# Optimization experiments

Hardware: AMD Instinct MI355X
Metric: run time of the kernel (lower is better)

Reference implementation:

```python
import jax, jax.numpy as jnp
import numpy as np

B, T, C = 2, 2048, 2048
N_HEAD, D_HEAD = 16, 128

def setup_inputs() -> dict:
    key = jax.random.key(0)
    k1, k2, k3 = jax.random.split(key, 3)
    x = jax.random.normal(k1, (B, T, C), dtype=jnp.float32)
    # lecun-normal-ish scaling for kernels
    W_attn = jax.random.normal(k2, (C, 3 * C), dtype=jnp.float32) * (1.0 / np.sqrt(C))
    W_proj = jax.random.normal(k3, (C, C), dtype=jnp.float32) * (1.0 / np.sqrt(C))
    return {"x": x, "W_attn": W_attn, "W_proj": W_proj}

def reference(x, W_attn, W_proj):
    Bx, Tx, Cx = x.shape
    # fused qkv projection: (B,T,C) @ (C,3C)
    qkv = x @ W_attn
    q, k, v = jnp.split(qkv, 3, axis=-1)
    # (B, H, T, Dh)
    q = q.reshape(Bx, Tx, N_HEAD, D_HEAD).transpose(0, 2, 1, 3)
    k = k.reshape(Bx, Tx, N_HEAD, D_HEAD).transpose(0, 2, 1, 3)
    v = v.reshape(Bx, Tx, N_HEAD, D_HEAD).transpose(0, 2, 1, 3)
    scale = 1.0 / jnp.sqrt(jnp.asarray(D_HEAD, dtype=x.dtype))
    att = jnp.einsum('bhqd,bhkd->bhqk', q, k) * scale  # (B,H,T,T)
    causal_mask = jnp.tril(jnp.ones((Tx, Tx), dtype=jnp.bool_))[None, None]
    att = jnp.where(causal_mask, att, -jnp.inf)
    att = jax.nn.softmax(att, axis=-1)
    y = jnp.einsum('bhqk,bhkd->bhqd', att, v)
    y = y.transpose(0, 2, 1, 3).reshape(Bx, Tx, Cx)
    return y @ W_proj
```

## Files before the change

kernel.cpp:

```cpp
#include <hip/hip_runtime.h>
#include <hip/hip_bf16.h>
#include <stdint.h>

#define AS1 __attribute__((address_space(1)))
#define AS3 __attribute__((address_space(3)))

typedef __bf16 bf16_t;
typedef __bf16 bf16x8 __attribute__((ext_vector_type(8)));
typedef float f32x4 __attribute__((ext_vector_type(4)));
typedef float f32x16 __attribute__((ext_vector_type(16)));

static constexpr int Bsz = 2, T = 2048, Cdim = 2048, NH = 16, DH = 128;
static constexpr int M  = Bsz * T;
static constexpr int N1 = 3 * Cdim;
static constexpr int K1 = Cdim;

__device__ __forceinline__ unsigned short f2bf(float f) {
  unsigned u = __float_as_uint(f);
  u += 0x7fffu + ((u >> 16) & 1u);
  return (unsigned short)(u >> 16);
}

__device__ __forceinline__ void gload_lds16(const bf16_t* g, void* l) {
  __builtin_amdgcn_global_load_lds((AS1 const void*)g, (AS3 void*)l, 16, 0, 0);
}

__device__ __forceinline__ float ex2(float x) {
  float r; asm("v_exp_f32 %0, %1" : "=v"(r) : "v"(x)); return r;
}
__device__ __forceinline__ unsigned pk2(float a, float b) {
  unsigned r; asm("v_cvt_pk_bf16_f32 %0, %1, %2" : "=v"(r) : "v"(a), "v"(b)); return r;
}

__global__ void cvt_kernel(const float* __restrict__ in, unsigned short* __restrict__ out, int n) {
  int i = (blockIdx.x * blockDim.x + threadIdx.x) * 4;
  if (i >= n) return;
  float4 v = *(const float4*)(in + i);
  ushort4 o;
  o.x = f2bf(v.x); o.y = f2bf(v.y); o.z = f2bf(v.z); o.w = f2bf(v.w);
  *(ushort4*)(out + i) = o;
}

__global__ void transpose_cvt_kernel(const float* __restrict__ in, unsigned short* __restrict__ out,
                                     int K, int N) {
  __shared__ float tile[32][33];
  int n0 = blockIdx.x * 32, k0 = blockIdx.y * 32;
  int tx = threadIdx.x, ty = threadIdx.y;
#pragma unroll
  for (int i = 0; i < 32; i += 8)
    tile[ty + i][tx] = in[(size_t)(k0 + ty + i) * N + n0 + tx];
  __syncthreads();
#pragma unroll
  for (int i = 0; i < 32; i += 8)
    out[(size_t)(n0 + ty + i) * K + k0 + tx] = f2bf(tile[tx][ty + i]);
}

__global__ void vtrans_kernel(const unsigned short* __restrict__ qkv, unsigned short* __restrict__ vt) {
  __shared__ unsigned short tile[32][33];
  int t0 = blockIdx.x * 32, d0 = blockIdx.y * 32, bh = blockIdx.z;
  int b = bh >> 4, h = bh & 15;
  int tx = threadIdx.x, ty = threadIdx.y;
  const unsigned short* src = qkv + (size_t)(b * T) * N1 + 2 * Cdim + h * DH;
#pragma unroll
  for (int i = 0; i < 32; i += 8)
    tile[ty + i][tx] = src[(size_t)(t0 + ty + i) * N1 + d0 + tx];
  __syncthreads();
  unsigned short* dst = vt + ((size_t)bh * DH + d0) * T + t0;
#pragma unroll
  for (int i = 0; i < 32; i += 8)
    dst[(size_t)(ty + i) * T + tx] = tile[tx][ty + i];
}

template <int OUT_BF16>
__global__ __launch_bounds__(512, 4) void gemm_p3(const bf16_t* __restrict__ A,
                                                  const bf16_t* __restrict__ BT,
                                                  void* __restrict__ Cp,
                                                  int Nn, int Kk) {
  constexpr int SLOT = 24576;
  __shared__ __align__(16) char ldsmem[3 * SLOT];
  char* ldsb = ldsmem;

  const int tid = threadIdx.x;
  const int wid = tid >> 6, lane = tid & 63;
  const int lq = lane & 15, lk = lane >> 4;
  const int wr = wid >> 2, wc = wid & 3;

  const int nwg = gridDim.x;
  const int bid = blockIdx.x;
  const int q8 = nwg >> 3;
  const int sw = (bid & 7) * q8 + (bid >> 3);
  const int gx = Nn >> 8;
  const int tn = sw % gx;
  const int tm = sw / gx;

  f32x4 acc[4][4] = {};

  int aoff[4], boff[4];
#pragma unroll
  for (int m = 0; m < 4; ++m) {
    int row = wr * 64 + m * 16 + lq;
    aoff[m] = row * 64 + ((lk * 16) ^ (((row >> 1) & 3) << 4));
  }
#pragma unroll
  for (int n = 0; n < 4; ++n) {
    int brow = wc * 64 + n * 16 + lq;
    boff[n] = 8192 + brow * 64 + ((lk * 16) ^ (((brow >> 1) & 3) << 4));
  }

  const int pA = wid * 1024 + lane * 16;
  const int arow = pA >> 6;
  const int acsw = (pA & 63) ^ (((arow >> 1) & 3) << 4);
  const bf16_t* Ags = A + (size_t)(tm * 128 + arow) * Kk + (acsw >> 1);

  const int pB0 = wid * 1024 + lane * 16;
  const int brow0 = pB0 >> 6;
  const int bcsw0 = (pB0 & 63) ^ (((brow0 >> 1) & 3) << 4);
  const bf16_t* Bgs0 = BT + (size_t)(tn * 256 + brow0) * Kk + (bcsw0 >> 1);

  const int pB1 = 8192 + wid * 1024 + lane * 16;
  const int brow1 = pB1 >> 6;
  const int bcsw1 = (pB1 & 63) ^ (((brow1 >> 1) & 3) << 4);
  const bf16_t* Bgs1 = BT + (size_t)(tn * 256 + brow1) * Kk + (bcsw1 >> 1);

  const int ldsA = wid * 1024;
  const int ldsB0 = 8192 + wid * 1024;
  const int ldsB1 = 16384 + wid * 1024;

  auto stage = [&](int kt, int slot) {
    char* db = ldsb + slot * SLOT;
    gload_lds16(Ags + (size_t)kt * 32, db + ldsA);
    gload_lds16(Bgs0 + (size_t)kt * 32, db + ldsB0);
    gload_lds16(Bgs1 + (size_t)kt * 32, db + ldsB1);
  };

  const int nk = Kk >> 5;

  stage(0, 0); stage(1, 1);
  asm volatile("s_waitcnt vmcnt(3)" ::: "memory");
  __builtin_amdgcn_s_barrier();

#define TILE_BODY(KT, SLOT0, SLOT2, STAGE_EN, VM)                                \
  {                                                                              \
    __builtin_amdgcn_sched_barrier(0);                                           \
    const char* sb = ldsb + (SLOT0) * SLOT;                                      \
    bf16x8 af[4], bfv[4];                                                        \
    _Pragma("unroll") for (int m = 0; m < 4; ++m)                                \
      af[m] = *(const bf16x8*)(sb + aoff[m]);                                    \
    _Pragma("unroll") for (int n = 0; n < 4; ++n)                                \
      bfv[n] = *(const bf16x8*)(sb + boff[n]);                                   \
    if (STAGE_EN) stage((KT) + 2, (SLOT2));                                      \
    __builtin_amdgcn_sched_barrier(0);                                           \
    __builtin_amdgcn_s_barrier();                                                \
    asm volatile("s_waitcnt lgkmcnt(0)" ::: "memory");                           \
    __builtin_amdgcn_sched_barrier(0);                                           \
    __builtin_amdgcn_s_setprio(1);                                               \
    _Pragma("unroll") for (int m = 0; m < 4; ++m)                                \
      _Pragma("unroll") for (int n = 0; n < 4; ++n)                              \
        acc[m][n] =                                                              \
            __builtin_amdgcn_mfma_f32_16x16x32_bf16(af[m], bfv[n], acc[m][n], 0, 0, 0); \
    __builtin_amdgcn_s_setprio(0);                                               \
    __builtin_amdgcn_sched_barrier(0);                                           \
    asm volatile("s_waitcnt vmcnt(" #VM ")" ::: "memory");                       \
    __builtin_amdgcn_s_barrier();                                                \
  }

  {
    int c0 = 0;
    for (int kt = 0; kt < nk - 2; ++kt) {
      const int c2 = (c0 >= 1) ? (c0 - 1) : (c0 + 2);
      TILE_BODY(kt, c0, c2, 1, 3);
      c0 = (c0 >= 2) ? 0 : (c0 + 1);
    }
    TILE_BODY(nk - 2, c0, 0, 0, 0);
    c0 = (c0 >= 2) ? 0 : (c0 + 1);
    TILE_BODY(nk - 1, c0, 0, 0, 0);
  }
#undef TILE_BODY

#pragma unroll
  for (int m = 0; m < 4; ++m)
#pragma unroll
    for (int n = 0; n < 4; ++n)
#pragma unroll
      for (int r = 0; r < 4; ++r) {
        int row = tm * 128 + wr * 64 + m * 16 + lk * 4 + r;
        int col = tn * 256 + wc * 64 + n * 16 + lq;
        if (OUT_BF16)
          ((unsigned short*)Cp)[(size_t)row * Nn + col] = f2bf(acc[m][n][r]);
        else
          ((float*)Cp)[(size_t)row * Nn + col] = acc[m][n][r];
      }
}

__global__ __launch_bounds__(512, 1) void attn_kernel(const bf16_t* __restrict__ qkv,
                                                      const bf16_t* __restrict__ vt,
                                                      unsigned short* __restrict__ y) {
  __shared__ __align__(16) char lds[65536];
  const int tid = threadIdx.x;
  const int wid = tid >> 6, lane = tid & 63;
  const int l31 = lane & 31, hi = lane >> 5;
  const int hi16 = hi << 4;
  const int bh = blockIdx.x;
  const int g = blockIdx.y;
  const int b = bh >> 4, h = bh & 15;
  const float SC2 = 0.12751879868954096f;

  const int grp = (wid < 4) ? g : (15 - g);
  const int qlo = grp * 128 + (wid & 3) * 32;
  const int qidx = qlo + l31;
  const int nt = 2 * (15 - g) + 2;
  const size_t rowbase = (size_t)(b * T) * N1;

  bf16x8 qf[8];
  {
    const bf16_t* Qg = qkv + rowbase + (size_t)qidx * N1 + h * DH + hi * 8;
#pragma unroll
    for (int kk = 0; kk < 8; ++kk) qf[kk] = *(const bf16x8*)(Qg + kk * 16);
  }

  const bf16_t* Kg0 = qkv + rowbase + Cdim + h * DH;
  const bf16_t* Vg0 = vt + (size_t)bh * DH * T;
  const int p0 = wid * 1024 + lane * 16;
  const int p1 = 8192 + wid * 1024 + lane * 16;
  const int kr0 = p0 >> 8, kr1 = p1 >> 8;
  const bf16_t* KsA = Kg0 + (size_t)kr0 * N1 + ((((p0 & 255) ^ ((kr0 & 15) << 4))) >> 1);
  const bf16_t* KsB = Kg0 + (size_t)kr1 * N1 + ((((p1 & 255) ^ ((kr1 & 15) << 4))) >> 1);
  const int vr0 = p0 >> 7, vr1 = p1 >> 7;
  const bf16_t* VsA = Vg0 + (size_t)vr0 * T + ((((p0 & 127) ^ ((vr0 & 7) << 4))) >> 1);
  const bf16_t* VsB = Vg0 + (size_t)vr1 * T + ((((p1 & 127) ^ ((vr1 & 7) << 4))) >> 1);
  const int dstoff = wid * 1024;

  auto stage = [&](int tt) {
    char* Kd = lds + (tt & 1) * 16384;
    char* Vd = lds + 32768 + (tt & 1) * 16384;
    const size_t ko = (size_t)(tt * 64) * N1;
    const int vo = tt * 64;
    gload_lds16(KsA + ko, Kd + dstoff);
    gload_lds16(KsB + ko, Kd + 8192 + dstoff);
    gload_lds16(VsA + vo, Vd + dstoff);
    gload_lds16(VsB + vo, Vd + 8192 + dstoff);
  };

  f32x16 oacc[4] = {};
  float mrow = -1e30f, lrow = 0.f;

  stage(0);
  asm volatile("s_waitcnt vmcnt(0)" ::: "memory");
  __builtin_amdgcn_s_barrier();

  for (int t = 0; t < nt; ++t) {
    const int kv0 = t * 64;
    if (t + 1 < nt) stage(t + 1);

    if (kv0 <= qlo + 31) {
      f32x16 s0 = {}, s1 = {};
      {
        const char* Kb = lds + (t & 1) * 16384;
        const char* krow0 = Kb + l31 * 256;
        const char* krow1 = Kb + (32 + l31) * 256;
        const int sw0 = (l31 & 15) << 4;
        const int sw1 = ((32 + l31) & 15) << 4;
#pragma unroll
        for (int kk = 0; kk < 8; ++kk) {
          bf16x8 kf0 = *(const bf16x8*)(krow0 + ((kk * 32 + hi16) ^ sw0));
          bf16x8 kf1 = *(const bf16x8*)(krow1 + ((kk * 32 + hi16) ^ sw1));
          s0 = __builtin_amdgcn_mfma_f32_32x32x16_bf16(kf0, qf[kk], s0, 0, 0, 0);
          s1 = __builtin_amdgcn_mfma_f32_32x32x16_bf16(kf1, qf[kk], s1, 0, 0, 0);
        }
      }
      float sv[32];
#pragma unroll
      for (int r = 0; r < 16; ++r) { sv[r] = s0[r]; sv[16 + r] = s1[r]; }
      if (kv0 + 63 > qlo) {
#pragma unroll
        for (int r = 0; r < 16; ++r) {
          const int roff = (r & 3) + 8 * (r >> 2);
          if (kv0 + roff + 4 * hi > qidx) sv[r] = -1e30f;
          if (kv0 + 32 + roff + 4 * hi > qidx) sv[16 + r] = -1e30f;
        }
      }
      float mx = sv[0];
#pragma unroll
      for (int i = 1; i < 32; ++i) mx = fmaxf(mx, sv[i]);
      mx = fmaxf(mx, __shfl_xor(mx, 32));
      const float mn = fmaxf(mrow, mx);
      const float osc = ex2((mrow - mn) * SC2);
      mrow = mn;
      const float mn2 = mn * SC2;
#pragma unroll
      for (int db = 0; db < 4; ++db) oacc[db] *= osc;
      float srow = 0.f;
#pragma unroll
      for (int i = 0; i < 32; ++i) {
        float p = ex2(fmaf(sv[i], SC2, -mn2));
        sv[i] = p;
        srow += p;
      }
      srow += __shfl_xor(srow, 32);
      lrow = lrow * osc + srow;
      bf16x8 pb[4];
#pragma unroll
      for (int s4 = 0; s4 < 4; ++s4) {
        const int base = (s4 >> 1) * 16 + (s4 & 1) * 8;
        unsigned x0 = pk2(sv[base + 0], sv[base + 1]);
        unsigned x1 = pk2(sv[base + 2], sv[base + 3]);
        unsigned y0 = pk2(sv[base + 4], sv[base + 5]);
        unsigned y1 = pk2(sv[base + 6], sv[base + 7]);
        unsigned e0 = (unsigned)__shfl_xor((int)(hi ? x0 : y0), 32);
        unsigned e1 = (unsigned)__shfl_xor((int)(hi ? x1 : y1), 32);
        union { unsigned u[4]; bf16x8 v; } pbu;
        pbu.u[0] = hi ? e0 : x0;
        pbu.u[1] = hi ? e1 : x1;
        pbu.u[2] = hi ? y0 : e0;
        pbu.u[3] = hi ? y1 : e1;
        pb[s4] = pbu.v;
      }
      {
        const char* Vb = lds + 32768 + (t & 1) * 16384;
#pragma unroll
        for (int db = 0; db < 4; ++db) {
          const int vrow = db * 32 + l31;
          const char* vr = Vb + vrow * 128;
          const int swv = (vrow & 7) << 4;
#pragma unroll
          for (int s4 = 0; s4 < 4; ++s4) {
            bf16x8 vf = *(const bf16x8*)(vr + ((s4 * 32 + hi16) ^ swv));
            oacc[db] = __builtin_amdgcn_mfma_f32_32x32x16_bf16(vf, pb[s4], oacc[db], 0, 0, 0);
          }
        }
      }
    }

    asm volatile("s_waitcnt vmcnt(0)" ::: "memory");
    __builtin_amdgcn_s_barrier();
  }

  const float inv = 1.0f / lrow;
  char* eb = lds + wid * 8192;
#pragma unroll
  for (int db = 0; db < 4; ++db)
#pragma unroll
    for (int r = 0; r < 16; ++r) {
      const int d = db * 32 + (r & 3) + 8 * (r >> 2) + 4 * hi;
      const int off = l31 * 256 + ((d * 2) ^ ((l31 & 15) << 4));
      *(unsigned short*)(eb + off) = f2bf(oacc[db][r] * inv);
    }
  asm volatile("s_waitcnt lgkmcnt(0)" ::: "memory");
  __builtin_amdgcn_sched_barrier(0);
  {
    unsigned short* yr = y + (size_t)(b * T + qlo + l31) * Cdim + h * DH;
#pragma unroll
    for (int rr = 0; rr < 8; ++rr) {
      const int c = hi * 8 + rr;
      bf16x8 v = *(const bf16x8*)(eb + l31 * 256 + ((c * 16) ^ ((l31 & 15) << 4)));
      *(bf16x8*)(yr + c * 8) = v;
    }
  }
}

extern "C" void kernel_launch(void* const* d_in, const int* in_sizes, int n_in,
                              void* d_out, int out_size, void* d_ws, size_t ws_size,
                              hipStream_t stream) {
  const float* x  = (const float*)d_in[0];
  const float* Wa = (const float*)d_in[1];
  const float* Wp = (const float*)d_in[2];
  float* out = (float*)d_out;
  char* ws = (char*)d_ws;

  size_t o0 = 0;
  size_t o1 = o0 + (size_t)M * K1 * 2;
  size_t o2 = o1 + (size_t)N1 * K1 * 2;
  size_t o3 = o2 + (size_t)M * N1 * 2;
  size_t o4 = o3 + (size_t)M * Cdim * 2;

  unsigned short* xb   = (unsigned short*)(ws + o0);
  unsigned short* WaT  = (unsigned short*)(ws + o1);
  unsigned short* qkvb = (unsigned short*)(ws + o2);
  unsigned short* yb   = (unsigned short*)(ws + o3);
  unsigned short* WpT  = (unsigned short*)(ws + o4);
  unsigned short* vtb  = xb;

  cvt_kernel<<<dim3((M * K1 / 4 + 255) / 256), dim3(256), 0, stream>>>(x, xb, M * K1);
  transpose_cvt_kernel<<<dim3(N1 / 32, K1 / 32), dim3(32, 8), 0, stream>>>(Wa, WaT, K1, N1);
  transpose_cvt_kernel<<<dim3(Cdim / 32, Cdim / 32), dim3(32, 8), 0, stream>>>(Wp, WpT, Cdim, Cdim);

  gemm_p3<1><<<dim3((M / 128) * (N1 / 256)), dim3(512), 0, stream>>>(
      (const bf16_t*)xb, (const bf16_t*)WaT, (void*)qkvb, N1, K1);

  vtrans_kernel<<<dim3(T / 32, DH / 32, Bsz * NH), dim3(32, 8), 0, stream>>>(qkvb, vtb);

  attn_kernel<<<dim3(Bsz * NH, 8), dim3(512), 0, stream>>>(
      (const bf16_t*)qkvb, (const bf16_t*)vtb, yb);

  gemm_p3<0><<<dim3((M / 128) * (Cdim / 256)), dim3(512), 0, stream>>>(
      (const bf16_t*)yb, (const bf16_t*)WpT, (void*)out, Cdim, K1);
}
```

Baseline: 249.6 us.

## Fuse preamble conversions, write V transposed from QKV GEMM, split GEMM tile body

The x conversion and the two weight transpose-conversions are merged into one preamble launch. The QKV GEMM epilogue now writes the V section already transposed, per batch and head, into the V region of qkv, so the separate vtrans kernel goes away and attention reads V^T straight from qkv. The GEMM inner tile is also split into two half-MFMA phases that interleave the A/B LDS reads and global-to-LDS staging, aiming for better overlap. This relies on the V region being laid out as D x T inside the N1-stride buffer, and it adds an extra barrier per k-step.

```diff
diff --git a/kernel.cpp b/kernel.cpp
--- a/kernel.cpp
+++ b/kernel.cpp
@@ -32,46 +32,41 @@
   unsigned r; asm("v_cvt_pk_bf16_f32 %0, %1, %2" : "=v"(r) : "v"(a), "v"(b)); return r;
 }
 
-__global__ void cvt_kernel(const float* __restrict__ in, unsigned short* __restrict__ out, int n) {
-  int i = (blockIdx.x * blockDim.x + threadIdx.x) * 4;
-  if (i >= n) return;
-  float4 v = *(const float4*)(in + i);
-  ushort4 o;
-  o.x = f2bf(v.x); o.y = f2bf(v.y); o.z = f2bf(v.z); o.w = f2bf(v.w);
-  *(ushort4*)(out + i) = o;
-}
-
-__global__ void transpose_cvt_kernel(const float* __restrict__ in, unsigned short* __restrict__ out,
-                                     int K, int N) {
+__global__ __launch_bounds__(256) void preamble_kernel(const float* __restrict__ x,
+                                                       const float* __restrict__ Wa,
+                                                       const float* __restrict__ Wp,
+                                                       unsigned short* __restrict__ xb,
+                                                       unsigned short* __restrict__ WaT,
+                                                       unsigned short* __restrict__ WpT) {
   __shared__ float tile[32][33];
-  int n0 = blockIdx.x * 32, k0 = blockIdx.y * 32;
-  int tx = threadIdx.x, ty = threadIdx.y;
+  const int blk = blockIdx.x;
+  const int tid = threadIdx.x;
+  if (blk < 8192) {
+    int i = blk * 1024 + tid * 4;
+    float4 v = *(const float4*)(x + i);
+    ushort4 o;
+    o.x = f2bf(v.x); o.y = f2bf(v.y); o.z = f2bf(v.z); o.w = f2bf(v.w);
+    *(ushort4*)(xb + i) = o;
+    return;
+  }
+  const float* in;
+  unsigned short* out;
+  int Nn, bi;
+  if (blk < 20480) { in = Wa; out = WaT; Nn = N1;   bi = blk - 8192;  }
+  else             { in = Wp; out = WpT; Nn = Cdim; bi = blk - 20480; }
+  const int ntiles = Nn >> 5;
+  const int n0 = (bi % ntiles) * 32, k0 = (bi / ntiles) * 32;
+  const int tx = tid & 31, ty = tid >> 5;
 #pragma unroll
   for (int i = 0; i < 32; i += 8)
-    tile[ty + i][tx] = in[(size_t)(k0 + ty + i) * N + n0 + tx];
+    tile[ty + i][tx] = in[(size_t)(k0 + ty + i) * Nn + n0 + tx];
   __syncthreads();
 #pragma unroll
   for (int i = 0; i < 32; i += 8)
-    out[(size_t)(n0 + ty + i) * K + k0 + tx] = f2bf(tile[tx][ty + i]);
-}
-
-__global__ void vtrans_kernel(const unsigned short* __restrict__ qkv, unsigned short* __restrict__ vt) {
-  __shared__ unsigned short tile[32][33];
-  int t0 = blockIdx.x * 32, d0 = blockIdx.y * 32, bh = blockIdx.z;
-  int b = bh >> 4, h = bh & 15;
-  int tx = threadIdx.x, ty = threadIdx.y;
-  const unsigned short* src = qkv + (size_t)(b * T) * N1 + 2 * Cdim + h * DH;
-#pragma unroll
-  for (int i = 0; i < 32; i += 8)
-    tile[ty + i][tx] = src[(size_t)(t0 + ty + i) * N1 + d0 + tx];
-  __syncthreads();
-  unsigned short* dst = vt + ((size_t)bh * DH + d0) * T + t0;
-#pragma unroll
-  for (int i = 0; i < 32; i += 8)
-    dst[(size_t)(ty + i) * T + tx] = tile[tx][ty + i];
-}
-
-template <int OUT_BF16>
+    out[(size_t)(n0 + ty + i) * K1 + k0 + tx] = f2bf(tile[tx][ty + i]);
+}
+
+template <int MODE>
 __global__ __launch_bounds__(512, 4) void gemm_p3(const bf16_t* __restrict__ A,
                                                   const bf16_t* __restrict__ BT,
                                                   void* __restrict__ Cp,
@@ -143,21 +138,43 @@
   {                                                                              \
     __builtin_amdgcn_sched_barrier(0);                                           \
     const char* sb = ldsb + (SLOT0) * SLOT;                                      \
-    bf16x8 af[4], bfv[4];                                                        \
-    _Pragma("unroll") for (int m = 0; m < 4; ++m)                                \
-      af[m] = *(const bf16x8*)(sb + aoff[m]);                                    \
+    bf16x8 af0, af1, af2, af3, bfv[4];                                           \
+    af0 = *(const bf16x8*)(sb + aoff[0]);                                        \
+    af1 = *(const bf16x8*)(sb + aoff[1]);                                        \
     _Pragma("unroll") for (int n = 0; n < 4; ++n)                                \
       bfv[n] = *(const bf16x8*)(sb + boff[n]);                                   \
-    if (STAGE_EN) stage((KT) + 2, (SLOT2));                                      \
+    if (STAGE_EN) {                                                              \
+      char* db = ldsb + (SLOT2) * SLOT;                                          \
+      gload_lds16(Ags + (size_t)((KT) + 2) * 32, db + ldsA);                     \
+      gload_lds16(Bgs0 + (size_t)((KT) + 2) * 32, db + ldsB0);                   \
+    }                                                                            \
     __builtin_amdgcn_sched_barrier(0);                                           \
     __builtin_amdgcn_s_barrier();                                                \
     asm volatile("s_waitcnt lgkmcnt(0)" ::: "memory");                           \
     __builtin_amdgcn_sched_barrier(0);                                           \
     __builtin_amdgcn_s_setprio(1);                                               \
-    _Pragma("unroll") for (int m = 0; m < 4; ++m)                                \
-      _Pragma("unroll") for (int n = 0; n < 4; ++n)                              \
-        acc[m][n] =                                                              \
-            __builtin_amdgcn_mfma_f32_16x16x32_bf16(af[m], bfv[n], acc[m][n], 0, 0, 0); \
+    _Pragma("unroll") for (int n = 0; n < 4; ++n) {                              \
+      acc[0][n] = __builtin_amdgcn_mfma_f32_16x16x32_bf16(af0, bfv[n], acc[0][n], 0, 0, 0); \
+      acc[1][n] = __builtin_amdgcn_mfma_f32_16x16x32_bf16(af1, bfv[n], acc[1][n], 0, 0, 0); \
+    }                                                                            \
+    __builtin_amdgcn_s_setprio(0);                                               \
+    __builtin_amdgcn_sched_barrier(0);                                           \
+    __builtin_amdgcn_s_barrier();                                                \
+    af2 = *(const bf16x8*)(sb + aoff[2]);                                        \
+    af3 = *(const bf16x8*)(sb + aoff[3]);                                        \
+    if (STAGE_EN) {                                                              \
+      char* db = ldsb + (SLOT2) * SLOT;                                          \
+      gload_lds16(Bgs1 + (size_t)((KT) + 2) * 32, db + ldsB1);                   \
+    }                                                                            \
+    __builtin_amdgcn_sched_barrier(0);                                           \
+    __builtin_amdgcn_s_barrier();                                                \
+    asm volatile("s_waitcnt lgkmcnt(0)" ::: "memory");                           \
+    __builtin_amdgcn_sched_barrier(0);                                           \
+    __builtin_amdgcn_s_setprio(1);                                               \
+    _Pragma("unroll") for (int n = 0; n < 4; ++n) {                              \
+      acc[2][n] = __builtin_amdgcn_mfma_f32_16x16x32_bf16(af2, bfv[n], acc[2][n], 0, 0, 0); \
+      acc[3][n] = __builtin_amdgcn_mfma_f32_16x16x32_bf16(af3, bfv[n], acc[3][n], 0, 0, 0); \
+    }                                                                            \
     __builtin_amdgcn_s_setprio(0);                                               \
     __builtin_amdgcn_sched_barrier(0);                                           \
     asm volatile("s_waitcnt vmcnt(" #VM ")" ::: "memory");                       \
@@ -177,23 +194,38 @@
   }
 #undef TILE_BODY
 
-#pragma unroll
-  for (int m = 0; m < 4; ++m)
-#pragma unroll
-    for (int n = 0; n < 4; ++n)
-#pragma unroll
-      for (int r = 0; r < 4; ++r) {
-        int row = tm * 128 + wr * 64 + m * 16 + lk * 4 + r;
-        int col = tn * 256 + wc * 64 + n * 16 + lq;
-        if (OUT_BF16)
-          ((unsigned short*)Cp)[(size_t)row * Nn + col] = f2bf(acc[m][n][r]);
-        else
-          ((float*)Cp)[(size_t)row * Nn + col] = acc[m][n][r];
-      }
+  if (MODE == 1 && tn >= 16) {
+    unsigned short* q16 = (unsigned short*)Cp;
+#pragma unroll
+    for (int m = 0; m < 4; ++m)
+#pragma unroll
+      for (int n = 0; n < 4; ++n) {
+        int row = tm * 128 + wr * 64 + m * 16 + lk * 4;
+        int b_ = row >> 11, t0 = row & 2047;
+        int c = tn * 256 - 4096 + wc * 64 + n * 16 + lq;
+        ushort4 o;
+        o.x = f2bf(acc[m][n][0]); o.y = f2bf(acc[m][n][1]);
+        o.z = f2bf(acc[m][n][2]); o.w = f2bf(acc[m][n][3]);
+        *(ushort4*)(q16 + (size_t)(b_ * 2048 + c) * N1 + 4096 + t0) = o;
+      }
+  } else {
+#pragma unroll
+    for (int m = 0; m < 4; ++m)
+#pragma unroll
+      for (int n = 0; n < 4; ++n)
+#pragma unroll
+        for (int r = 0; r < 4; ++r) {
+          int row = tm * 128 + wr * 64 + m * 16 + lk * 4 + r;
+          int col = tn * 256 + wc * 64 + n * 16 + lq;
+          if (MODE == 1)
+            ((unsigned short*)Cp)[(size_t)row * Nn + col] = f2bf(acc[m][n][r]);
+          else
+            ((float*)Cp)[(size_t)row * Nn + col] = acc[m][n][r];
+        }
+  }
 }
 
 __global__ __launch_bounds__(512, 1) void attn_kernel(const bf16_t* __restrict__ qkv,
-                                                      const bf16_t* __restrict__ vt,
                                                       unsigned short* __restrict__ y) {
   __shared__ __align__(16) char lds[65536];
   const int tid = threadIdx.x;
@@ -219,15 +251,15 @@
   }
 
   const bf16_t* Kg0 = qkv + rowbase + Cdim + h * DH;
-  const bf16_t* Vg0 = vt + (size_t)bh * DH * T;
+  const bf16_t* Vg0 = qkv + (size_t)(b * 2048 + h * DH) * N1 + 2 * Cdim;
   const int p0 = wid * 1024 + lane * 16;
   const int p1 = 8192 + wid * 1024 + lane * 16;
   const int kr0 = p0 >> 8, kr1 = p1 >> 8;
   const bf16_t* KsA = Kg0 + (size_t)kr0 * N1 + ((((p0 & 255) ^ ((kr0 & 15) << 4))) >> 1);
   const bf16_t* KsB = Kg0 + (size_t)kr1 * N1 + ((((p1 & 255) ^ ((kr1 & 15) << 4))) >> 1);
   const int vr0 = p0 >> 7, vr1 = p1 >> 7;
-  const bf16_t* VsA = Vg0 + (size_t)vr0 * T + ((((p0 & 127) ^ ((vr0 & 7) << 4))) >> 1);
-  const bf16_t* VsB = Vg0 + (size_t)vr1 * T + ((((p1 & 127) ^ ((vr1 & 7) << 4))) >> 1);
+  const bf16_t* VsA = Vg0 + (size_t)vr0 * N1 + ((((p0 & 127) ^ ((vr0 & 7) << 4))) >> 1);
+  const bf16_t* VsB = Vg0 + (size_t)vr1 * N1 + ((((p1 & 127) ^ ((vr1 & 7) << 4))) >> 1);
   const int dstoff = wid * 1024;
 
   auto stage = [&](int tt) {
@@ -378,19 +410,14 @@
   unsigned short* qkvb = (unsigned short*)(ws + o2);
   unsigned short* yb   = (unsigned short*)(ws + o3);
   unsigned short* WpT  = (unsigned short*)(ws + o4);
-  unsigned short* vtb  = xb;
-
-  cvt_kernel<<<dim3((M * K1 / 4 + 255) / 256), dim3(256), 0, stream>>>(x, xb, M * K1);
-  transpose_cvt_kernel<<<dim3(N1 / 32, K1 / 32), dim3(32, 8), 0, stream>>>(Wa, WaT, K1, N1);
-  transpose_cvt_kernel<<<dim3(Cdim / 32, Cdim / 32), dim3(32, 8), 0, stream>>>(Wp, WpT, Cdim, Cdim);
+
+  preamble_kernel<<<dim3(24576), dim3(256), 0, stream>>>(x, Wa, Wp, xb, WaT, WpT);
 
   gemm_p3<1><<<dim3((M / 128) * (N1 / 256)), dim3(512), 0, stream>>>(
       (const bf16_t*)xb, (const bf16_t*)WaT, (void*)qkvb, N1, K1);
 
-  vtrans_kernel<<<dim3(T / 32, DH / 32, Bsz * NH), dim3(32, 8), 0, stream>>>(qkvb, vtb);
-
   attn_kernel<<<dim3(Bsz * NH, 8), dim3(512), 0, stream>>>(
-      (const bf16_t*)qkvb, (const bf16_t*)vtb, yb);
+      (const bf16_t*)qkvb, yb);
 
   gemm_p3<0><<<dim3((M / 128) * (Cdim / 256)), dim3(512), 0, stream>>>(
       (const bf16_t*)yb, (const bf16_t*)WpT, (void*)out, Cdim, K1);
```

Measured after the change: 241.0 us. 3.4% less time.
